# Optimization experiments

Hardware: AMD Instinct MI355X
Metric: run time of the kernel (lower is better)

Reference implementation:

```python
import jax, jax.numpy as jnp
import numpy as np

N, TP, E = 8, 2048, 4096
S = 8            # 2**spatial_dim
C = 64           # sqrt(embed_dim)
T = TP * S       # 16384
V = 16           # num_vocab


def setup_inputs() -> dict:
    key = jax.random.key(0)
    ks = jax.random.split(key, 9)
    x = jax.random.normal(ks[0], (N, TP, E), dtype=jnp.float32)
    value = jax.random.randint(ks[1], (N, T), 0, 4, dtype=jnp.int64)
    depth = jnp.sort(jax.random.randint(ks[2], (N, T), 0, 16, dtype=jnp.int64), axis=1)
    pos = jax.random.randint(ks[3], (N, T, 3), 0, 32, dtype=jnp.int64)
    # ConvTranspose1d(E, C, kernel=S, stride=S): weight [E, C, S]
    W1 = jax.random.normal(ks[4], (E, C, S), dtype=jnp.float32) / np.sqrt(E)
    b1 = jax.random.normal(ks[5], (C,), dtype=jnp.float32) * 0.01
    # ConvTranspose1d(C, 1, kernel=S, stride=S): weight [C, 1, S]
    W2 = jax.random.normal(ks[6], (C, 1, S), dtype=jnp.float32) / np.sqrt(C)
    b2 = jax.random.normal(ks[7], (1,), dtype=jnp.float32) * 0.01
    # Linear(1, V+1, bias=False): weight [V+1, 1]
    W3 = jax.random.normal(ks[8], (V + 1, 1), dtype=jnp.float32)
    return {"x": x, "value": value, "depth": depth, "pos": pos,
            "W1": W1, "b1": b1, "W2": W2, "b2": b2, "W3": W3}


def reference(x, value, depth, pos, W1, b1, W2, b2, W3):
    n, tp, e = x.shape
    s = W1.shape[2]
    t = value.shape[1]  # = tp * s
    posn = jnp.arange(t)
    # Truncate each value sequence at argmax(depth); pad_sequence pads with 0.
    idx = jnp.argmax(depth, axis=1)                      # [N]
    val_pad = jnp.where(posn[None, :] < idx[:, None], value, 0)  # [N, T]
    # deconv_1: stride == kernel -> non-overlapping expansion
    x1 = jnp.einsum('nte,ecs->ntsc', x, W1).reshape(n, t, -1) + b1  # [N, T, C]
    # Per-sample masked gather (val==2), compacted to front, zero-padded
    mask = val_pad == 2                                   # [N, T]
    order = jnp.argsort(jnp.logical_not(mask), axis=1, stable=True)  # True first
    y = jnp.take_along_axis(x1, order[:, :, None], axis=1)           # [N, T, C]
    counts = mask.sum(axis=1)                             # [N]
    y = jnp.where((posn[None, :] < counts[:, None])[:, :, None], y, 0.0)
    # deconv_2: [N, T, C] -> [N, T*S, 1]
    y2 = jnp.einsum('ntc,cs->nts', y, W2[:, 0, :]).reshape(n, t * s, 1) + b2
    # linear (no bias): [N, T*S, V+1]
    return y2 @ W3.T
```

## Files before the change

kernel.cpp:

```cpp
#include <hip/hip_runtime.h>

#define N_    8
#define TP_   2048
#define E_    4096
#define S_    8
#define C_    64
#define T_    16384
#define TS_   131072
#define OUTW  17
#define OUT_ELEMS 17825792
#define F4_PER_N 557056
#define F4_TOTAL 4456448
#define KSTEPS 128
#define GEMM_BLOCKS 512
#define FILL_BLOCKS 4352
#define MPREP_BLOCKS 256

typedef __attribute__((ext_vector_type(8))) short short8;
typedef __attribute__((ext_vector_type(4))) float float4v;

static __device__ __forceinline__ unsigned short f2bf(float f) {
    unsigned int u = __builtin_bit_cast(unsigned int, f);
    u += 0x7FFFu + ((u >> 16) & 1u);
    return (unsigned short)(u >> 16);
}
static __device__ __forceinline__ float bf2f(unsigned short h) {
    return __builtin_bit_cast(float, (unsigned int)h << 16);
}

__global__ __launch_bounds__(256) void prep_compact_kernel(
    const float* __restrict__ W1, const float* __restrict__ b1,
    const float* __restrict__ W2, const float* __restrict__ b2,
    const int* __restrict__ value, const int* __restrict__ depth,
    unsigned short* __restrict__ Mhi, unsigned short* __restrict__ Mlo,
    float* __restrict__ K2,
    int* __restrict__ cnt_ns, int* __restrict__ cnt_total,
    int* __restrict__ tile_counter, int* __restrict__ tiles,
    int* __restrict__ sel_tp, int* __restrict__ sel_j)
{
    const int tid = threadIdx.x;
    const int b   = blockIdx.x;

    if (b < 64) {
        __shared__ int idx_sh;
        __shared__ unsigned int wsum[4];
        const int g = b;
        const int n = g >> 3;
        const int s = g & 7;
        const int lane = tid & 63;
        const int wv   = tid >> 6;

        const int* d = depth + (size_t)n * T_;
        if (tid < 64) {
            int maxv = d[T_ - 1];
            int lower = 0, upper = T_ - 1;
            for (int rnd = 0; rnd < 3; ++rnd) {
                int span = upper - lower;
                int step = (span + 63) >> 6;
                if (step < 1) step = 1;
                int p = lower + lane * step;
                if (p > upper) p = upper;
                unsigned long long bb = __ballot(d[p] == maxv);
                int f = __ffsll((long long)bb) - 1;
                int nu = lower + f * step; if (nu > upper) nu = upper;
                int nl = (f == 0) ? lower : lower + (f - 1) * step + 1;
                if (nl > nu) nl = nu;
                lower = nl; upper = nu;
            }
            if (lane == 0) idx_sh = lower;
        }
        __syncthreads();
        const int idx = idx_sh;
        const int4* val4 = (const int4*)(value + (size_t)n * T_);

        const int b4 = tid * 16;
        unsigned int packed = 0;
        for (int i = 0; i < 16; ++i) {
            int4 v = val4[b4 + i];
            int t = (b4 + i) * 4;
            if (t + 0 < idx && v.x == 2) { packed += 0x10000u; if (((t + 0) & 7) == s) packed += 1u; }
            if (t + 1 < idx && v.y == 2) { packed += 0x10000u; if (((t + 1) & 7) == s) packed += 1u; }
            if (t + 2 < idx && v.z == 2) { packed += 0x10000u; if (((t + 2) & 7) == s) packed += 1u; }
            if (t + 3 < idx && v.w == 2) { packed += 0x10000u; if (((t + 3) & 7) == s) packed += 1u; }
        }
        unsigned int inc = packed;
#pragma unroll
        for (int off = 1; off < 64; off <<= 1) {
            unsigned int u = __shfl_up((int)inc, off, 64);
            if (lane >= off) inc += u;
        }
        if (lane == 63) wsum[wv] = inc;
        __syncthreads();
        unsigned int woff = 0;
        for (int ww = 0; ww < wv; ++ww) woff += wsum[ww];
        unsigned int excl = woff + inc - packed;
        int any_rank = (int)(excl >> 16);
        int s_rank   = (int)(excl & 0xFFFFu);
        for (int i = 0; i < 16; ++i) {
            int4 v = val4[b4 + i];
            int vv[4] = { v.x, v.y, v.z, v.w };
            int t = (b4 + i) * 4;
#pragma unroll
            for (int e = 0; e < 4; ++e) {
                int tt = t + e;
                if (tt < idx && vv[e] == 2) {
                    if ((tt & 7) == s) {
                        sel_tp[g * 2048 + s_rank] = tt >> 3;
                        sel_j [g * 2048 + s_rank] = any_rank;
                        ++s_rank;
                    }
                    ++any_rank;
                }
            }
        }
        if (tid == 255) {
            unsigned int tot = woff + inc;
            int cnt = (int)(tot & 0xFFFFu);
            cnt_ns[g] = cnt;
            if (s == 0) cnt_total[n] = (int)(tot >> 16);
            int ntl = (cnt + 63) >> 6;
            int base = atomicAdd(tile_counter, ntl);
            for (int i = 0; i < ntl; ++i) tiles[base + i] = (g << 8) | i;
        }
        return;
    }

    __shared__ float W1t[16 * 512];
    __shared__ float W2s[512];

    if (b == 64 && tid < 8) {
        int s2 = tid;
        float acc = b2[0];
        for (int c = 0; c < C_; ++c) acc += b1[c] * W2[c * S_ + s2];
        K2[s2] = acc;
    }

    const int kk    = b - 64;
    const int kstep = kk >> 1;
    const int h     = kk & 1;
    const int k0    = kstep * 32 + h * 16;

    for (int i = tid; i < 512; i += 256) W2s[i] = W2[i];
    {
        const float4* src = (const float4*)(W1 + (size_t)k0 * 512);
        float4* dst = (float4*)W1t;
        for (int i = tid; i < 16 * 128; i += 256) dst[i] = src[i];
    }
    __syncthreads();

    const int s    = tid >> 5;
    const int lsub = tid & 31;
    const int lane = h * 32 + lsub;
    const int qq   = lsub >> 4;
    const int s2   = lane & 15;

    float accj[8] = {0.f,0.f,0.f,0.f,0.f,0.f,0.f,0.f};
    if (s2 < 8) {
        for (int c = 0; c < C_; ++c) {
            float w2 = W2s[c * 8 + s2];
            int base = c * 8 + s;
#pragma unroll
            for (int j = 0; j < 8; ++j)
                accj[j] += W1t[(qq * 8 + j) * 512 + base] * w2;
        }
    }
    size_t o = ((size_t)(s * KSTEPS + kstep) * 64 + lane) * 8;
#pragma unroll
    for (int j = 0; j < 8; ++j) {
        unsigned short hi = f2bf(accj[j]);
        unsigned short lo = f2bf(accj[j] - bf2f(hi));
        Mhi[o + j] = hi;
        Mlo[o + j] = lo;
    }
}

__global__ __launch_bounds__(256) void main_kernel(
    const float* __restrict__ x,
    const unsigned short* __restrict__ Mhi, const unsigned short* __restrict__ Mlo,
    const int* __restrict__ tile_counter, const int* __restrict__ tiles,
    const int* __restrict__ cnt_ns, const int* __restrict__ sel_tp,
    const int* __restrict__ sel_j, const float* __restrict__ K2,
    const float* __restrict__ W3, const float* __restrict__ b2,
    const int* __restrict__ cnt_total, float* __restrict__ out)
{
    const int tid = threadIdx.x;

    if (blockIdx.x >= GEMM_BLOCKS) {
        __shared__ float pat[136];
        if (tid < 136) pat[tid] = b2[0] * W3[tid % OUTW];
        __syncthreads();
        const int fb = blockIdx.x - GEMM_BLOCKS;
#pragma unroll
        for (int it = 0; it < 4; ++it) {
            int i4 = fb * 1024 + it * 256 + tid;
            int n   = i4 / F4_PER_N;
            int rem = i4 - n * F4_PER_N;
            int j   = rem / 34;
            if (j >= cnt_total[n]) {
                int o = (rem - j * 34) * 4;
                float4 v = { pat[o], pat[o + 1], pat[o + 2], pat[o + 3] };
                *(float4*)&out[(size_t)i4 * 4] = v;
            }
        }
        return;
    }

    __shared__ int tp_l[64], j_l[64];
    __shared__ float y2s[64][8];
    __shared__ float W3s[OUTW];
    __shared__ float K2s[S_];

    if (tid < OUTW) W3s[tid] = W3[tid];
    if (tid < S_)   K2s[tid] = K2[tid];

    const int ntile = *tile_counter;
    const int lane = tid & 63;
    const int w    = tid >> 6;
    const int m    = lane & 15;
    const int q    = lane >> 4;

    for (int ti = blockIdx.x; ti < ntile; ti += GEMM_BLOCKS) {
        const int ent = tiles[ti];
        const int g = ent >> 8;
        const int n = g >> 3;
        const int s = g & 7;
        const int m0 = (ent & 255) * 64;
        const int rows = min(64, cnt_ns[g] - m0);

        __syncthreads();
        if (tid < 64) {
            int tp = 0, j = 0;
            if (tid < rows) {
                tp = sel_tp[g * 2048 + m0 + tid];
                j  = sel_j [g * 2048 + m0 + tid];
            }
            tp_l[tid] = tp;
            j_l[tid]  = j;
        }
        __syncthreads();

        const float* arow = x + ((size_t)n * TP_ + tp_l[w * 16 + m]) * E_ + q * 8;
        const unsigned short* bh = Mhi + ((size_t)s * KSTEPS * 64 + lane) * 8;
        const unsigned short* bl = Mlo + ((size_t)s * KSTEPS * 64 + lane) * 8;

        float4v acc = {0.f, 0.f, 0.f, 0.f};

        float4 A00 = *(const float4*)(arow);
        float4 A01 = *(const float4*)(arow + 4);
        short8 Bh0 = *(const short8*)(bh);
        short8 Bl0 = *(const short8*)(bl);
        float4 A10 = *(const float4*)(arow + 32);
        float4 A11 = *(const float4*)(arow + 36);
        short8 Bh1 = *(const short8*)(bh + 512);
        short8 Bl1 = *(const short8*)(bl + 512);

#define STEP(P, A0, A1, BH, BL)                                                \
        {                                                                      \
            short8 av;                                                         \
            av[0] = (short)f2bf(A0.x); av[1] = (short)f2bf(A0.y);              \
            av[2] = (short)f2bf(A0.z); av[3] = (short)f2bf(A0.w);              \
            av[4] = (short)f2bf(A1.x); av[5] = (short)f2bf(A1.y);              \
            av[6] = (short)f2bf(A1.z); av[7] = (short)f2bf(A1.w);              \
            short8 bhc = BH, blc = BL;                                         \
            if (ks + 2 + P < KSTEPS) {                                         \
                const float* ap = arow + (size_t)(ks + 2 + P) * 32;            \
                A0 = *(const float4*)(ap);                                     \
                A1 = *(const float4*)(ap + 4);                                 \
                BH = *(const short8*)(bh + (size_t)(ks + 2 + P) * 512);        \
                BL = *(const short8*)(bl + (size_t)(ks + 2 + P) * 512);        \
            }                                                                  \
            acc = __builtin_amdgcn_mfma_f32_16x16x32_bf16(av, bhc, acc, 0, 0, 0); \
            acc = __builtin_amdgcn_mfma_f32_16x16x32_bf16(av, blc, acc, 0, 0, 0); \
        }

        for (int ks = 0; ks < KSTEPS; ks += 2) {
            STEP(0, A00, A01, Bh0, Bl0)
            STEP(1, A10, A11, Bh1, Bl1)
        }
#undef STEP

        if (m < 8) {
#pragma unroll
            for (int rr = 0; rr < 4; ++rr)
                y2s[w * 16 + q * 4 + rr][m] = acc[rr] + K2s[m];
        }
        __syncthreads();

        for (int task = tid; task < 64 * 34; task += 256) {
            int row = task / 34;
            int f   = task - row * 34;
            if (row < rows) {
                float4 v;
                float* vp = (float*)&v;
#pragma unroll
                for (int e = 0; e < 4; ++e) {
                    int idx = f * 4 + e;
                    int s2  = (idx * 241) >> 12;
                    int vi  = idx - s2 * OUTW;
                    vp[e] = y2s[row][s2] * W3s[vi];
                }
                *(float4*)&out[((size_t)n * TS_ + (size_t)j_l[row] * S_) * OUTW + f * 4] = v;
            }
        }
    }
}

extern "C" void kernel_launch(void* const* d_in, const int* in_sizes, int n_in,
                              void* d_out, int out_size, void* d_ws, size_t ws_size,
                              hipStream_t stream) {
    const float* x     = (const float*)d_in[0];
    const int*   value = (const int*)d_in[1];
    const int*   depth = (const int*)d_in[2];
    const float* W1    = (const float*)d_in[4];
    const float* b1    = (const float*)d_in[5];
    const float* W2    = (const float*)d_in[6];
    const float* b2    = (const float*)d_in[7];
    const float* W3    = (const float*)d_in[8];
    float* out = (float*)d_out;

    unsigned short* Mhi = (unsigned short*)d_ws;
    unsigned short* Mlo = Mhi + 8 * KSTEPS * 64 * 8;
    float* K2          = (float*)(Mlo + 8 * KSTEPS * 64 * 8);
    int* tile_counter  = (int*)(K2 + 8);
    int* cnt_ns        = tile_counter + 1;
    int* cnt_total     = cnt_ns + 64;
    int* tiles         = cnt_total + 8;
    int* sel_tp        = tiles + 2048;
    int* sel_j         = sel_tp + 64 * 2048;

    hipMemsetAsync(tile_counter, 0, sizeof(int), stream);

    prep_compact_kernel<<<64 + MPREP_BLOCKS, 256, 0, stream>>>(
        W1, b1, W2, b2, value, depth, Mhi, Mlo, K2,
        cnt_ns, cnt_total, tile_counter, tiles, sel_tp, sel_j);

    main_kernel<<<GEMM_BLOCKS + FILL_BLOCKS, 256, 0, stream>>>(
        x, Mhi, Mlo, tile_counter, tiles, cnt_ns, sel_tp, sel_j,
        K2, W3, b2, cnt_total, out);
}
```

Baseline: 456.1 us.

## Split K across two waves with 16-row tiles and packed bf16 conversion

```diff
diff --git a/kernel.cpp b/kernel.cpp
--- a/kernel.cpp
+++ b/kernel.cpp
@@ -12,7 +12,7 @@
 #define F4_PER_N 557056
 #define F4_TOTAL 4456448
 #define KSTEPS 128
-#define GEMM_BLOCKS 512
+#define GEMM_BLOCKS 2048
 #define FILL_BLOCKS 4352
 #define MPREP_BLOCKS 256
 
@@ -26,6 +26,11 @@
 }
 static __device__ __forceinline__ float bf2f(unsigned short h) {
     return __builtin_bit_cast(float, (unsigned int)h << 16);
+}
+static __device__ __forceinline__ unsigned int cvt_pk(float lo, float hi) {
+    unsigned int r;
+    asm("v_cvt_pk_bf16_f32 %0, %1, %2" : "=v"(r) : "v"(lo), "v"(hi));
+    return r;
 }
 
 __global__ __launch_bounds__(256) void prep_compact_kernel(
@@ -118,7 +123,7 @@
             int cnt = (int)(tot & 0xFFFFu);
             cnt_ns[g] = cnt;
             if (s == 0) cnt_total[n] = (int)(tot >> 16);
-            int ntl = (cnt + 63) >> 6;
+            int ntl = (cnt + 15) >> 4;
             int base = atomicAdd(tile_counter, ntl);
             for (int i = 0; i < ntl; ++i) tiles[base + i] = (g << 8) | i;
         }
@@ -174,7 +179,7 @@
     }
 }
 
-__global__ __launch_bounds__(256) void main_kernel(
+__global__ __launch_bounds__(128) void main_kernel(
     const float* __restrict__ x,
     const unsigned short* __restrict__ Mhi, const unsigned short* __restrict__ Mlo,
     const int* __restrict__ tile_counter, const int* __restrict__ tiles,
@@ -187,12 +192,12 @@
 
     if (blockIdx.x >= GEMM_BLOCKS) {
         __shared__ float pat[136];
-        if (tid < 136) pat[tid] = b2[0] * W3[tid % OUTW];
+        for (int i = tid; i < 136; i += 128) pat[i] = b2[0] * W3[i % OUTW];
         __syncthreads();
         const int fb = blockIdx.x - GEMM_BLOCKS;
 #pragma unroll
-        for (int it = 0; it < 4; ++it) {
-            int i4 = fb * 1024 + it * 256 + tid;
+        for (int it = 0; it < 8; ++it) {
+            int i4 = fb * 1024 + it * 128 + tid;
             int n   = i4 / F4_PER_N;
             int rem = i4 - n * F4_PER_N;
             int j   = rem / 34;
@@ -205,8 +210,9 @@
         return;
     }
 
-    __shared__ int tp_l[64], j_l[64];
-    __shared__ float y2s[64][8];
+    __shared__ int tp_l[16], j_l[16];
+    __shared__ float pacc[2][64][4];
+    __shared__ float y2s[16][8];
     __shared__ float W3s[OUTW];
     __shared__ float K2s[S_];
 
@@ -224,11 +230,11 @@
         const int g = ent >> 8;
         const int n = g >> 3;
         const int s = g & 7;
-        const int m0 = (ent & 255) * 64;
-        const int rows = min(64, cnt_ns[g] - m0);
-
-        __syncthreads();
-        if (tid < 64) {
+        const int m0 = (ent & 255) * 16;
+        const int rows = min(16, cnt_ns[g] - m0);
+
+        __syncthreads();
+        if (tid < 16) {
             int tp = 0, j = 0;
             if (tid < rows) {
                 tp = sel_tp[g * 2048 + m0 + tid];
@@ -239,9 +245,9 @@
         }
         __syncthreads();
 
-        const float* arow = x + ((size_t)n * TP_ + tp_l[w * 16 + m]) * E_ + q * 8;
-        const unsigned short* bh = Mhi + ((size_t)s * KSTEPS * 64 + lane) * 8;
-        const unsigned short* bl = Mlo + ((size_t)s * KSTEPS * 64 + lane) * 8;
+        const float* arow = x + ((size_t)n * TP_ + tp_l[m]) * E_ + w * 2048 + q * 8;
+        const unsigned short* bh = Mhi + ((size_t)(s * KSTEPS + w * 64) * 64 + lane) * 8;
+        const unsigned short* bl = Mlo + ((size_t)(s * KSTEPS + w * 64) * 64 + lane) * 8;
 
         float4v acc = {0.f, 0.f, 0.f, 0.f};
 
@@ -256,13 +262,14 @@
 
 #define STEP(P, A0, A1, BH, BL)                                                \
         {                                                                      \
-            short8 av;                                                         \
-            av[0] = (short)f2bf(A0.x); av[1] = (short)f2bf(A0.y);              \
-            av[2] = (short)f2bf(A0.z); av[3] = (short)f2bf(A0.w);              \
-            av[4] = (short)f2bf(A1.x); av[5] = (short)f2bf(A1.y);              \
-            av[6] = (short)f2bf(A1.z); av[7] = (short)f2bf(A1.w);              \
+            int4 aw;                                                           \
+            aw.x = (int)cvt_pk(A0.x, A0.y);                                    \
+            aw.y = (int)cvt_pk(A0.z, A0.w);                                    \
+            aw.z = (int)cvt_pk(A1.x, A1.y);                                    \
+            aw.w = (int)cvt_pk(A1.z, A1.w);                                    \
+            short8 av = __builtin_bit_cast(short8, aw);                        \
             short8 bhc = BH, blc = BL;                                         \
-            if (ks + 2 + P < KSTEPS) {                                         \
+            if (ks + 2 + P < 64) {                                             \
                 const float* ap = arow + (size_t)(ks + 2 + P) * 32;            \
                 A0 = *(const float4*)(ap);                                     \
                 A1 = *(const float4*)(ap + 4);                                 \
@@ -273,20 +280,24 @@
             acc = __builtin_amdgcn_mfma_f32_16x16x32_bf16(av, blc, acc, 0, 0, 0); \
         }
 
-        for (int ks = 0; ks < KSTEPS; ks += 2) {
+        for (int ks = 0; ks < 64; ks += 2) {
             STEP(0, A00, A01, Bh0, Bl0)
             STEP(1, A10, A11, Bh1, Bl1)
         }
 #undef STEP
 
-        if (m < 8) {
-#pragma unroll
-            for (int rr = 0; rr < 4; ++rr)
-                y2s[w * 16 + q * 4 + rr][m] = acc[rr] + K2s[m];
-        }
-        __syncthreads();
-
-        for (int task = tid; task < 64 * 34; task += 256) {
+        *(float4v*)&pacc[w][lane][0] = acc;
+        __syncthreads();
+        {
+            int row = tid >> 3;
+            int s2  = tid & 7;
+            int ln  = ((row >> 2) << 4) | s2;
+            int rr  = row & 3;
+            y2s[row][s2] = K2s[s2] + pacc[0][ln][rr] + pacc[1][ln][rr];
+        }
+        __syncthreads();
+
+        for (int task = tid; task < 16 * 34; task += 128) {
             int row = task / 34;
             int f   = task - row * 34;
             if (row < rows) {
@@ -325,7 +336,7 @@
     int* cnt_ns        = tile_counter + 1;
     int* cnt_total     = cnt_ns + 64;
     int* tiles         = cnt_total + 8;
-    int* sel_tp        = tiles + 2048;
+    int* sel_tp        = tiles + 8192;
     int* sel_j         = sel_tp + 64 * 2048;
 
     hipMemsetAsync(tile_counter, 0, sizeof(int), stream);
@@ -334,7 +345,7 @@
         W1, b1, W2, b2, value, depth, Mhi, Mlo, K2,
         cnt_ns, cnt_total, tile_counter, tiles, sel_tp, sel_j);
 
-    main_kernel<<<GEMM_BLOCKS + FILL_BLOCKS, 256, 0, stream>>>(
+    main_kernel<<<GEMM_BLOCKS + FILL_BLOCKS, 128, 0, stream>>>(
         x, Mhi, Mlo, tile_counter, tiles, cnt_ns, sel_tp, sel_j,
         K2, W3, b2, cnt_total, out);
 }
```

Result: no change. 457.1 us (+0.2%).

## Gather unique x rows once and compute all 8 sub-positions per row

Applied to the files above, without the earlier changes.

```diff
diff --git a/kernel.cpp b/kernel.cpp
--- a/kernel.cpp
+++ b/kernel.cpp
@@ -14,7 +14,6 @@
 #define KSTEPS 128
 #define GEMM_BLOCKS 512
 #define FILL_BLOCKS 4352
-#define MPREP_BLOCKS 256
 
 typedef __attribute__((ext_vector_type(8))) short short8;
 typedef __attribute__((ext_vector_type(4))) float float4v;
@@ -26,6 +25,11 @@
 }
 static __device__ __forceinline__ float bf2f(unsigned short h) {
     return __builtin_bit_cast(float, (unsigned int)h << 16);
+}
+static __device__ __forceinline__ unsigned int cvt_pk(float lo, float hi) {
+    unsigned int r;
+    asm("v_cvt_pk_bf16_f32 %0, %1, %2" : "=v"(r) : "v"(lo), "v"(hi));
+    return r;
 }
 
 __global__ __launch_bounds__(256) void prep_compact_kernel(
@@ -34,19 +38,17 @@
     const int* __restrict__ value, const int* __restrict__ depth,
     unsigned short* __restrict__ Mhi, unsigned short* __restrict__ Mlo,
     float* __restrict__ K2,
-    int* __restrict__ cnt_ns, int* __restrict__ cnt_total,
+    int* __restrict__ ucnt, int* __restrict__ cnt_total,
     int* __restrict__ tile_counter, int* __restrict__ tiles,
-    int* __restrict__ sel_tp, int* __restrict__ sel_j)
+    int* __restrict__ urow_tp, int* __restrict__ uslot)
 {
     const int tid = threadIdx.x;
     const int b   = blockIdx.x;
 
-    if (b < 64) {
+    if (b < 8) {
         __shared__ int idx_sh;
         __shared__ unsigned int wsum[4];
-        const int g = b;
-        const int n = g >> 3;
-        const int s = g & 7;
+        const int n = b;
         const int lane = tid & 63;
         const int wv   = tid >> 6;
 
@@ -74,15 +76,22 @@
         const int4* val4 = (const int4*)(value + (size_t)n * T_);
 
         const int b4 = tid * 16;
-        unsigned int packed = 0;
+        unsigned long long mask = 0ull;
         for (int i = 0; i < 16; ++i) {
             int4 v = val4[b4 + i];
             int t = (b4 + i) * 4;
-            if (t + 0 < idx && v.x == 2) { packed += 0x10000u; if (((t + 0) & 7) == s) packed += 1u; }
-            if (t + 1 < idx && v.y == 2) { packed += 0x10000u; if (((t + 1) & 7) == s) packed += 1u; }
-            if (t + 2 < idx && v.z == 2) { packed += 0x10000u; if (((t + 2) & 7) == s) packed += 1u; }
-            if (t + 3 < idx && v.w == 2) { packed += 0x10000u; if (((t + 3) & 7) == s) packed += 1u; }
-        }
+            int lt = t - tid * 64;
+            if (t + 0 < idx && v.x == 2) mask |= 1ull << (lt + 0);
+            if (t + 1 < idx && v.y == 2) mask |= 1ull << (lt + 1);
+            if (t + 2 < idx && v.z == 2) mask |= 1ull << (lt + 2);
+            if (t + 3 < idx && v.w == 2) mask |= 1ull << (lt + 3);
+        }
+        int selc = __popcll(mask);
+        int uc = 0;
+#pragma unroll
+        for (int p = 0; p < 8; ++p) if ((mask >> (8 * p)) & 255ull) ++uc;
+
+        unsigned int packed = ((unsigned int)selc << 16) | (unsigned int)uc;
         unsigned int inc = packed;
 #pragma unroll
         for (int off = 1; off < 64; off <<= 1) {
@@ -94,77 +103,69 @@
         unsigned int woff = 0;
         for (int ww = 0; ww < wv; ++ww) woff += wsum[ww];
         unsigned int excl = woff + inc - packed;
-        int any_rank = (int)(excl >> 16);
-        int s_rank   = (int)(excl & 0xFFFFu);
-        for (int i = 0; i < 16; ++i) {
-            int4 v = val4[b4 + i];
-            int vv[4] = { v.x, v.y, v.z, v.w };
-            int t = (b4 + i) * 4;
-#pragma unroll
-            for (int e = 0; e < 4; ++e) {
-                int tt = t + e;
-                if (tt < idx && vv[e] == 2) {
-                    if ((tt & 7) == s) {
-                        sel_tp[g * 2048 + s_rank] = tt >> 3;
-                        sel_j [g * 2048 + s_rank] = any_rank;
-                        ++s_rank;
-                    }
-                    ++any_rank;
-                }
+        int j = (int)(excl >> 16);
+        int u = (int)(excl & 0xFFFFu);
+#pragma unroll
+        for (int p = 0; p < 8; ++p) {
+            unsigned int bmask = (unsigned int)((mask >> (8 * p)) & 255ull);
+            if (bmask) {
+                urow_tp[n * 2048 + u] = tid * 8 + p;
+                int* slot = &uslot[(n * 2048 + u) * 8];
+#pragma unroll
+                for (int s = 0; s < 8; ++s)
+                    slot[s] = ((bmask >> s) & 1u) ? j++ : -1;
+                ++u;
             }
         }
         if (tid == 255) {
             unsigned int tot = woff + inc;
-            int cnt = (int)(tot & 0xFFFFu);
-            cnt_ns[g] = cnt;
-            if (s == 0) cnt_total[n] = (int)(tot >> 16);
-            int ntl = (cnt + 63) >> 6;
+            cnt_total[n] = (int)(tot >> 16);
+            int un = (int)(tot & 0xFFFFu);
+            ucnt[n] = un;
+            int ntl = (un + 31) >> 5;
             int base = atomicAdd(tile_counter, ntl);
-            for (int i = 0; i < ntl; ++i) tiles[base + i] = (g << 8) | i;
+            for (int i = 0; i < ntl; ++i) tiles[base + i] = (n << 8) | i;
         }
         return;
     }
 
-    __shared__ float W1t[16 * 512];
+    __shared__ float W1t[32 * 512];
     __shared__ float W2s[512];
 
-    if (b == 64 && tid < 8) {
+    if (b == 8 && tid < 8) {
         int s2 = tid;
         float acc = b2[0];
         for (int c = 0; c < C_; ++c) acc += b1[c] * W2[c * S_ + s2];
         K2[s2] = acc;
     }
 
-    const int kk    = b - 64;
-    const int kstep = kk >> 1;
-    const int h     = kk & 1;
-    const int k0    = kstep * 32 + h * 16;
+    const int kstep = b - 8;
 
     for (int i = tid; i < 512; i += 256) W2s[i] = W2[i];
     {
-        const float4* src = (const float4*)(W1 + (size_t)k0 * 512);
+        const float4* src = (const float4*)(W1 + (size_t)kstep * 32 * 512);
         float4* dst = (float4*)W1t;
-        for (int i = tid; i < 16 * 128; i += 256) dst[i] = src[i];
+        for (int i = tid; i < 32 * 128; i += 256) dst[i] = src[i];
     }
     __syncthreads();
 
-    const int s    = tid >> 5;
-    const int lsub = tid & 31;
-    const int lane = h * 32 + lsub;
-    const int qq   = lsub >> 4;
-    const int s2   = lane & 15;
+    const int ct   = tid >> 6;
+    const int l    = tid & 63;
+    const int q    = l >> 4;
+    const int c15  = l & 15;
+    const int scol = ct * 16 + c15;
+    const int s    = scol >> 3;
+    const int s2   = scol & 7;
 
     float accj[8] = {0.f,0.f,0.f,0.f,0.f,0.f,0.f,0.f};
-    if (s2 < 8) {
-        for (int c = 0; c < C_; ++c) {
-            float w2 = W2s[c * 8 + s2];
-            int base = c * 8 + s;
-#pragma unroll
-            for (int j = 0; j < 8; ++j)
-                accj[j] += W1t[(qq * 8 + j) * 512 + base] * w2;
-        }
-    }
-    size_t o = ((size_t)(s * KSTEPS + kstep) * 64 + lane) * 8;
+    for (int c = 0; c < C_; ++c) {
+        float w2 = W2s[c * 8 + s2];
+        int base = c * 8 + s;
+#pragma unroll
+        for (int j = 0; j < 8; ++j)
+            accj[j] += W1t[(q * 8 + j) * 512 + base] * w2;
+    }
+    size_t o = ((size_t)(ct * KSTEPS + kstep) * 64 + l) * 8;
 #pragma unroll
     for (int j = 0; j < 8; ++j) {
         unsigned short hi = f2bf(accj[j]);
@@ -178,8 +179,8 @@
     const float* __restrict__ x,
     const unsigned short* __restrict__ Mhi, const unsigned short* __restrict__ Mlo,
     const int* __restrict__ tile_counter, const int* __restrict__ tiles,
-    const int* __restrict__ cnt_ns, const int* __restrict__ sel_tp,
-    const int* __restrict__ sel_j, const float* __restrict__ K2,
+    const int* __restrict__ ucnt, const int* __restrict__ urow_tp,
+    const int* __restrict__ uslot, const float* __restrict__ K2,
     const float* __restrict__ W3, const float* __restrict__ b2,
     const int* __restrict__ cnt_total, float* __restrict__ out)
 {
@@ -205,8 +206,11 @@
         return;
     }
 
-    __shared__ int tp_l[64], j_l[64];
-    __shared__ float y2s[64][8];
+    __shared__ int tp_l[32];
+    __shared__ int js[32][8];
+    __shared__ float y64[32][68];
+    __shared__ int olist[256];
+    __shared__ int ocnt;
     __shared__ float W3s[OUTW];
     __shared__ float K2s[S_];
 
@@ -215,92 +219,117 @@
 
     const int ntile = *tile_counter;
     const int lane = tid & 63;
-    const int w    = tid >> 6;
+    const int wid  = tid >> 6;
+    const int wr   = wid >> 1;
+    const int wc   = wid & 1;
     const int m    = lane & 15;
     const int q    = lane >> 4;
 
     for (int ti = blockIdx.x; ti < ntile; ti += GEMM_BLOCKS) {
         const int ent = tiles[ti];
-        const int g = ent >> 8;
-        const int n = g >> 3;
-        const int s = g & 7;
-        const int m0 = (ent & 255) * 64;
-        const int rows = min(64, cnt_ns[g] - m0);
-
-        __syncthreads();
-        if (tid < 64) {
-            int tp = 0, j = 0;
-            if (tid < rows) {
-                tp = sel_tp[g * 2048 + m0 + tid];
-                j  = sel_j [g * 2048 + m0 + tid];
-            }
-            tp_l[tid] = tp;
-            j_l[tid]  = j;
-        }
-        __syncthreads();
-
-        const float* arow = x + ((size_t)n * TP_ + tp_l[w * 16 + m]) * E_ + q * 8;
-        const unsigned short* bh = Mhi + ((size_t)s * KSTEPS * 64 + lane) * 8;
-        const unsigned short* bl = Mlo + ((size_t)s * KSTEPS * 64 + lane) * 8;
-
-        float4v acc = {0.f, 0.f, 0.f, 0.f};
-
-        float4 A00 = *(const float4*)(arow);
-        float4 A01 = *(const float4*)(arow + 4);
-        short8 Bh0 = *(const short8*)(bh);
-        short8 Bl0 = *(const short8*)(bl);
-        float4 A10 = *(const float4*)(arow + 32);
-        float4 A11 = *(const float4*)(arow + 36);
-        short8 Bh1 = *(const short8*)(bh + 512);
-        short8 Bl1 = *(const short8*)(bl + 512);
-
-#define STEP(P, A0, A1, BH, BL)                                                \
+        const int n  = ent >> 8;
+        const int m0 = (ent & 255) * 32;
+        const int rows = min(32, ucnt[n] - m0);
+
+        __syncthreads();
+        if (tid < 32)
+            tp_l[tid] = (tid < rows) ? urow_tp[n * 2048 + m0 + tid] : 0;
+        {
+            int r = tid >> 3, s = tid & 7;
+            js[r][s] = (r < rows) ? uslot[(n * 2048 + m0 + r) * 8 + s] : -1;
+        }
+        if (tid == 0) ocnt = 0;
+        __syncthreads();
+
+        const float* arow = x + ((size_t)n * TP_ + tp_l[wr * 16 + m]) * E_ + q * 8;
+        const int ct0 = wc * 2, ct1 = wc * 2 + 1;
+        const unsigned short* bh0 = Mhi + ((size_t)ct0 * KSTEPS * 64 + lane) * 8;
+        const unsigned short* bl0 = Mlo + ((size_t)ct0 * KSTEPS * 64 + lane) * 8;
+        const unsigned short* bh1 = Mhi + ((size_t)ct1 * KSTEPS * 64 + lane) * 8;
+        const unsigned short* bl1 = Mlo + ((size_t)ct1 * KSTEPS * 64 + lane) * 8;
+
+        float4v acc0 = {0.f, 0.f, 0.f, 0.f};
+        float4v acc1 = {0.f, 0.f, 0.f, 0.f};
+
+        float4 A0a = *(const float4*)(arow);
+        float4 A1a = *(const float4*)(arow + 4);
+        short8 H0a = *(const short8*)(bh0);
+        short8 L0a = *(const short8*)(bl0);
+        short8 H1a = *(const short8*)(bh1);
+        short8 L1a = *(const short8*)(bl1);
+        float4 A0b = *(const float4*)(arow + 32);
+        float4 A1b = *(const float4*)(arow + 36);
+        short8 H0b = *(const short8*)(bh0 + 512);
+        short8 L0b = *(const short8*)(bl0 + 512);
+        short8 H1b = *(const short8*)(bh1 + 512);
+        short8 L1b = *(const short8*)(bl1 + 512);
+
+#define STEP(P, A0, A1, H0, L0, H1, L1)                                        \
         {                                                                      \
-            short8 av;                                                         \
-            av[0] = (short)f2bf(A0.x); av[1] = (short)f2bf(A0.y);              \
-            av[2] = (short)f2bf(A0.z); av[3] = (short)f2bf(A0.w);              \
-            av[4] = (short)f2bf(A1.x); av[5] = (short)f2bf(A1.y);              \
-            av[6] = (short)f2bf(A1.z); av[7] = (short)f2bf(A1.w);              \
-            short8 bhc = BH, blc = BL;                                         \
+            int4 aw;                                                           \
+            aw.x = (int)cvt_pk(A0.x, A0.y);                                    \
+            aw.y = (int)cvt_pk(A0.z, A0.w);                                    \
+            aw.z = (int)cvt_pk(A1.x, A1.y);                                    \
+            aw.w = (int)cvt_pk(A1.z, A1.w);                                    \
+            short8 av = __builtin_bit_cast(short8, aw);                        \
+            short8 h0 = H0, l0 = L0, h1 = H1, l1 = L1;                         \
             if (ks + 2 + P < KSTEPS) {                                         \
                 const float* ap = arow + (size_t)(ks + 2 + P) * 32;            \
+                size_t bo = (size_t)(ks + 2 + P) * 512;                        \
                 A0 = *(const float4*)(ap);                                     \
                 A1 = *(const float4*)(ap + 4);                                 \
-                BH = *(const short8*)(bh + (size_t)(ks + 2 + P) * 512);        \
-                BL = *(const short8*)(bl + (size_t)(ks + 2 + P) * 512);        \
+                H0 = *(const short8*)(bh0 + bo);                               \
+                L0 = *(const short8*)(bl0 + bo);                               \
+                H1 = *(const short8*)(bh1 + bo);                               \
+                L1 = *(const short8*)(bl1 + bo);                               \
             }                                                                  \
-            acc = __builtin_amdgcn_mfma_f32_16x16x32_bf16(av, bhc, acc, 0, 0, 0); \
-            acc = __builtin_amdgcn_mfma_f32_16x16x32_bf16(av, blc, acc, 0, 0, 0); \
+            acc0 = __builtin_amdgcn_mfma_f32_16x16x32_bf16(av, h0, acc0, 0, 0, 0); \
+            acc0 = __builtin_amdgcn_mfma_f32_16x16x32_bf16(av, l0, acc0, 0, 0, 0); \
+            acc1 = __builtin_amdgcn_mfma_f32_16x16x32_bf16(av, h1, acc1, 0, 0, 0); \
+            acc1 = __builtin_amdgcn_mfma_f32_16x16x32_bf16(av, l1, acc1, 0, 0, 0); \
         }
 
         for (int ks = 0; ks < KSTEPS; ks += 2) {
-            STEP(0, A00, A01, Bh0, Bl0)
-            STEP(1, A10, A11, Bh1, Bl1)
+            STEP(0, A0a, A1a, H0a, L0a, H1a, L1a)
+            STEP(1, A0b, A1b, H0b, L0b, H1b, L1b)
         }
 #undef STEP
 
-        if (m < 8) {
-#pragma unroll
-            for (int rr = 0; rr < 4; ++rr)
-                y2s[w * 16 + q * 4 + rr][m] = acc[rr] + K2s[m];
-        }
-        __syncthreads();
-
-        for (int task = tid; task < 64 * 34; task += 256) {
-            int row = task / 34;
-            int f   = task - row * 34;
-            if (row < rows) {
-                float4 v;
-                float* vp = (float*)&v;
-#pragma unroll
-                for (int e = 0; e < 4; ++e) {
-                    int idx = f * 4 + e;
-                    int s2  = (idx * 241) >> 12;
-                    int vi  = idx - s2 * OUTW;
-                    vp[e] = y2s[row][s2] * W3s[vi];
-                }
-                *(float4*)&out[((size_t)n * TS_ + (size_t)j_l[row] * S_) * OUTW + f * 4] = v;
-            }
+#pragma unroll
+        for (int rr = 0; rr < 4; ++rr) {
+            y64[wr * 16 + q * 4 + rr][ct0 * 16 + m] = acc0[rr];
+            y64[wr * 16 + q * 4 + rr][ct1 * 16 + m] = acc1[rr];
+        }
+        __syncthreads();
+
+        {
+            int r = tid >> 3, s = tid & 7;
+            int j = js[r][s];
+            if (r < rows && j >= 0) {
+                int k = atomicAdd(&ocnt, 1);
+                olist[k] = (j << 8) | (r << 3) | s;
+            }
+        }
+        __syncthreads();
+
+        const int oc = ocnt;
+        for (int task = tid; task < oc * 34; task += 256) {
+            int e34 = task / 34;
+            int f   = task - e34 * 34;
+            int pk  = olist[e34];
+            int j   = pk >> 8;
+            int r   = (pk >> 3) & 31;
+            int s   = pk & 7;
+            float4 v;
+            float* vp = (float*)&v;
+#pragma unroll
+            for (int e = 0; e < 4; ++e) {
+                int idx = f * 4 + e;
+                int s2  = (idx * 241) >> 12;
+                int vi  = idx - s2 * OUTW;
+                vp[e] = (y64[r][s * 8 + s2] + K2s[s2]) * W3s[vi];
+            }
+            *(float4*)&out[((size_t)n * TS_ + (size_t)j * S_) * OUTW + f * 4] = v;
         }
     }
 }
@@ -319,22 +348,22 @@
     float* out = (float*)d_out;
 
     unsigned short* Mhi = (unsigned short*)d_ws;
-    unsigned short* Mlo = Mhi + 8 * KSTEPS * 64 * 8;
-    float* K2          = (float*)(Mlo + 8 * KSTEPS * 64 * 8);
+    unsigned short* Mlo = Mhi + 4 * KSTEPS * 64 * 8;
+    float* K2          = (float*)(Mlo + 4 * KSTEPS * 64 * 8);
     int* tile_counter  = (int*)(K2 + 8);
-    int* cnt_ns        = tile_counter + 1;
-    int* cnt_total     = cnt_ns + 64;
+    int* ucnt          = tile_counter + 1;
+    int* cnt_total     = ucnt + 8;
     int* tiles         = cnt_total + 8;
-    int* sel_tp        = tiles + 2048;
-    int* sel_j         = sel_tp + 64 * 2048;
+    int* urow_tp       = tiles + 512;
+    int* uslot         = urow_tp + 8 * 2048;
 
     hipMemsetAsync(tile_counter, 0, sizeof(int), stream);
 
-    prep_compact_kernel<<<64 + MPREP_BLOCKS, 256, 0, stream>>>(
+    prep_compact_kernel<<<8 + KSTEPS, 256, 0, stream>>>(
         W1, b1, W2, b2, value, depth, Mhi, Mlo, K2,
-        cnt_ns, cnt_total, tile_counter, tiles, sel_tp, sel_j);
+        ucnt, cnt_total, tile_counter, tiles, urow_tp, uslot);
 
     main_kernel<<<GEMM_BLOCKS + FILL_BLOCKS, 256, 0, stream>>>(
-        x, Mhi, Mlo, tile_counter, tiles, cnt_ns, sel_tp, sel_j,
+        x, Mhi, Mlo, tile_counter, tiles, ucnt, urow_tp, uslot,
         K2, W3, b2, cnt_total, out);
 }
```

New measurement: 452.3 us. Within noise of the previous version (-0.8%).
